# Kernel optimization log

Hardware: AMD Instinct MI355X
Metric: run time of the kernel (lower is better)

## Reference

```python
import jax, jax.numpy as jnp
import numpy as np

N = 100000   # nodes
E = 1600000  # edges
IN_CH = 128
EDGE_DIM = 16
HEADS = 4
OUT_CH = 16
NEG_SLOPE = 0.2


def setup_inputs() -> dict:
    key = jax.random.key(0)
    ks = jax.random.split(key, 12)
    HC = HEADS * OUT_CH
    inp = {
        "x": jax.random.normal(ks[0], (N, IN_CH), dtype=jnp.float32),
        "edge_index": jax.random.randint(ks[1], (2, E), 0, N, dtype=jnp.int32),
        "edge_attr": jax.random.normal(ks[2], (E, EDGE_DIM), dtype=jnp.float32),
        # linear layer params (W stored as [in, out] so y = x @ W + b)
        "W_src": jax.random.normal(ks[3], (IN_CH, HC), dtype=jnp.float32) / np.sqrt(IN_CH),
        "b_src": jnp.zeros((HC,), dtype=jnp.float32),
        "W_dst": jax.random.normal(ks[4], (IN_CH, HC), dtype=jnp.float32) / np.sqrt(IN_CH),
        "b_dst": jnp.zeros((HC,), dtype=jnp.float32),
        "W_edge": jax.random.normal(ks[5], (EDGE_DIM, HC), dtype=jnp.float32) / np.sqrt(EDGE_DIM),
        "b_edge": jnp.zeros((HC,), dtype=jnp.float32),
        # attention vectors [1, heads, out_channels]
        "att_src": jax.random.normal(ks[6], (1, HEADS, OUT_CH), dtype=jnp.float32) * 0.1,
        "att_dst": jax.random.normal(ks[7], (1, HEADS, OUT_CH), dtype=jnp.float32) * 0.1,
        "att_edge": jax.random.normal(ks[8], (1, HEADS, OUT_CH), dtype=jnp.float32) * 0.1,
    }
    return inp


def _segment_softmax(alpha, seg, num_segments):
    # alpha: [E, H]; softmax over edges sharing the same dst node (seg).
    m = jax.ops.segment_max(alpha, seg, num_segments=num_segments)
    m = jnp.where(jnp.isfinite(m), m, 0.0)  # empty segments -> -inf; neutralize
    a = jnp.exp(alpha - m[seg])
    s = jax.ops.segment_sum(a, seg, num_segments=num_segments)
    return a / (s[seg] + 1e-16)


def reference(x, edge_index, edge_attr, W_src, b_src, W_dst, b_dst,
              W_edge, b_edge, att_src, att_dst, att_edge):
    n = x.shape[0]
    src_idx, dst_idx = edge_index[0], edge_index[1]

    src = (x @ W_src + b_src).reshape(n, HEADS, OUT_CH)        # [N,H,C]
    dst = (x @ W_dst + b_dst).reshape(n, HEADS, OUT_CH)        # [N,H,C]
    edge_feat = (edge_attr @ W_edge + b_edge).reshape(-1, HEADS, OUT_CH)  # [E,H,C]

    alpha_src = jnp.sum(src * att_src, axis=-1)[src_idx]       # [E,H]
    alpha_dst = jnp.sum(dst * att_dst, axis=-1)[dst_idx]       # [E,H]
    alpha_edge = jnp.sum(edge_feat * att_edge, axis=-1)        # [E,H]

    alpha = alpha_src + alpha_dst + alpha_edge
    alpha = jnp.where(alpha >= 0, alpha, NEG_SLOPE * alpha)    # leaky_relu(0.2)
    alpha = _segment_softmax(alpha, dst_idx, n)                # [E,H]
    # dropout is identity in eval mode

    msg = src[src_idx] * alpha[..., None]                      # [E,H,C]
    out = jax.ops.segment_sum(msg, dst_idx, num_segments=n)    # [N,H,C]
    return out.reshape(n, HEADS * OUT_CH)
```

## Files before the change

### kernel.cpp

```cpp
#include <hip/hip_runtime.h>


#define N_NODES 100000
#define N_EDGES 1600000
#define SCAN_B 1024
#define SCAN_NBLK ((N_NODES + SCAN_B - 1) / SCAN_B)

typedef float f32x4 __attribute__((ext_vector_type(4)));
typedef int   i32x4 __attribute__((ext_vector_type(4)));

static __device__ __forceinline__ unsigned int f2bf(float f) {
    unsigned int u = __float_as_uint(f);
    return (u + 0x7fffu + ((u >> 16) & 1u)) >> 16;
}
static __device__ __forceinline__ float bf2f(unsigned int bits16) {
    return __uint_as_float(bits16 << 16);
}

__global__ __launch_bounds__(256) void k_node_proj(
    const float* __restrict__ x, const float* __restrict__ Wsrc,
    const float* __restrict__ bsrc, const float* __restrict__ Wdst,
    const float* __restrict__ bdst, const float* __restrict__ att_src,
    const float* __restrict__ att_dst, unsigned short* __restrict__ spbf,
    float* __restrict__ alpha_sn, float* __restrict__ alpha_dn)
{
    __shared__ float wS[128 * 64];
    __shared__ float wD[128 * 64];
    const int tid = threadIdx.x;
    const int nbase = blockIdx.x * 32;

    {
        const f32x4* s4 = (const f32x4*)Wsrc;
        const f32x4* d4 = (const f32x4*)Wdst;
        f32x4* ls = (f32x4*)wS;
        f32x4* ld = (f32x4*)wD;
#pragma unroll
        for (int i = 0; i < 8; ++i) {
            ls[tid + i * 256] = s4[tid + i * 256];
            ld[tid + i * 256] = d4[tid + i * 256];
        }
    }
    __syncthreads();

    const int col = tid & 63;
    const int g = tid >> 6;
    const float* xrow = x + (size_t)(nbase + g * 8) * 128;

    float accS[8], accD[8];
#pragma unroll
    for (int i = 0; i < 8; ++i) { accS[i] = 0.f; accD[i] = 0.f; }

    for (int k4 = 0; k4 < 128; k4 += 4) {
        f32x4 xv[8];
#pragma unroll
        for (int i = 0; i < 8; ++i)
            xv[i] = *(const f32x4*)&xrow[i * 128 + k4];
#pragma unroll
        for (int kk = 0; kk < 4; ++kk) {
            const float wsv = wS[(k4 + kk) * 64 + col];
            const float wdv = wD[(k4 + kk) * 64 + col];
#pragma unroll
            for (int i = 0; i < 8; ++i) {
                accS[i] = fmaf(xv[i][kk], wsv, accS[i]);
                accD[i] = fmaf(xv[i][kk], wdv, accD[i]);
            }
        }
    }

    const float bs = bsrc[col], bd = bdst[col];
    const float as_ = att_src[col], ad_ = att_dst[col];
    const int h = col >> 4;
#pragma unroll
    for (int i = 0; i < 8; ++i) {
        const int n = nbase + g * 8 + i;
        float vS = accS[i] + bs;
        float vD = accD[i] + bd;
        spbf[(size_t)n * 64 + col] = (unsigned short)f2bf(vS);
        float t1 = vS * as_;
        float t2 = vD * ad_;
#pragma unroll
        for (int off = 8; off >= 1; off >>= 1) {
            t1 += __shfl_xor(t1, off, 16);
            t2 += __shfl_xor(t2, off, 16);
        }
        if ((col & 15) == 0) {
            alpha_sn[n * 4 + h] = t1;
            alpha_dn[n * 4 + h] = t2;
        }
    }
}

__global__ void k_prep(const float* __restrict__ We, const float* __restrict__ be,
                       const float* __restrict__ att_e, float* __restrict__ V)
{
    const int t = threadIdx.x;
    const int k = t >> 2, h = t & 3;
    float acc = 0.f;
    for (int c = 0; c < 16; ++c)
        acc += We[k * 64 + h * 16 + c] * att_e[h * 16 + c];
    V[k * 4 + h] = acc;
    if (t < 4) {
        float b = 0.f;
        for (int c = 0; c < 16; ++c)
            b += be[t * 16 + c] * att_e[t * 16 + c];
        V[64 + t] = b;
    }
}

__global__ __launch_bounds__(256) void k_hist(const int* __restrict__ ei,
                                               int* __restrict__ cnt)
{
    const int e = blockIdx.x * 256 + threadIdx.x;
    if (e >= N_EDGES) return;
    atomicAdd(&cnt[ei[N_EDGES + e]], 1);
}

__global__ __launch_bounds__(256) void k_scan_part(const int* __restrict__ cnt,
                                                    int* __restrict__ partial)
{
    __shared__ int red[4];
    const int t = threadIdx.x;
    const int base = blockIdx.x * SCAN_B + t * 4;
    int s = 0;
#pragma unroll
    for (int i = 0; i < 4; ++i) {
        const int idx = base + i;
        if (idx < N_NODES) s += cnt[idx];
    }
#pragma unroll
    for (int off = 32; off >= 1; off >>= 1)
        s += __shfl_xor(s, off, 64);
    if ((t & 63) == 0) red[t >> 6] = s;
    __syncthreads();
    if (t == 0)
        partial[blockIdx.x] = red[0] + red[1] + red[2] + red[3];
}

__global__ __launch_bounds__(128) void k_scan_top(int* __restrict__ partial)
{
    __shared__ int sums[128];
    const int t = threadIdx.x;
    sums[t] = (t < SCAN_NBLK) ? partial[t] : 0;
    __syncthreads();
#pragma unroll
    for (int off = 1; off < 128; off <<= 1) {
        int v = (t >= off) ? sums[t - off] : 0;
        __syncthreads();
        sums[t] += v;
        __syncthreads();
    }
    if (t < SCAN_NBLK) partial[t] = (t == 0) ? 0 : sums[t - 1];
}

__global__ __launch_bounds__(256) void k_scan_down(
    const int* __restrict__ cnt, const int* __restrict__ partial,
    int* __restrict__ row_start, int* __restrict__ cursor)
{
    __shared__ int tsum[256];
    const int t = threadIdx.x;
    const int base = blockIdx.x * SCAN_B + t * 4;
    int c[4];
#pragma unroll
    for (int i = 0; i < 4; ++i) {
        const int idx = base + i;
        c[i] = (idx < N_NODES) ? cnt[idx] : 0;
    }
    const int tot = c[0] + c[1] + c[2] + c[3];
    tsum[t] = tot;
    __syncthreads();
#pragma unroll
    for (int off = 1; off < 256; off <<= 1) {
        int v = (t >= off) ? tsum[t - off] : 0;
        __syncthreads();
        tsum[t] += v;
        __syncthreads();
    }
    int run = partial[blockIdx.x] + ((t == 0) ? 0 : tsum[t - 1]);
#pragma unroll
    for (int i = 0; i < 4; ++i) {
        const int idx = base + i;
        if (idx < N_NODES) {
            row_start[idx] = run;
            cursor[idx] = run;
        }
        run += c[i];
    }
    if (blockIdx.x == 0 && t == 0)
        row_start[N_NODES] = N_EDGES;
}

__global__ __launch_bounds__(256) void k_fill(
    const int* __restrict__ ei, const float* __restrict__ ea,
    const float* __restrict__ V, const float* __restrict__ alpha_sn,
    const float* __restrict__ alpha_dn, int* __restrict__ cursor,
    int4* __restrict__ rec)
{
    __shared__ float Vs[68];
    if (threadIdx.x < 68) Vs[threadIdx.x] = V[threadIdx.x];
    __syncthreads();

    const int e = blockIdx.x * 256 + threadIdx.x;
    if (e >= N_EDGES) return;
    const int src = ei[e];
    const int dst = ei[N_EDGES + e];

    const f32x4* ea4 = (const f32x4*)(ea + (size_t)e * 16);
    float ek[16];
    {
        f32x4 c0 = __builtin_nontemporal_load(ea4 + 0);
        f32x4 c1 = __builtin_nontemporal_load(ea4 + 1);
        f32x4 c2 = __builtin_nontemporal_load(ea4 + 2);
        f32x4 c3 = __builtin_nontemporal_load(ea4 + 3);
        ek[0]=c0.x; ek[1]=c0.y; ek[2]=c0.z; ek[3]=c0.w;
        ek[4]=c1.x; ek[5]=c1.y; ek[6]=c1.z; ek[7]=c1.w;
        ek[8]=c2.x; ek[9]=c2.y; ek[10]=c2.z; ek[11]=c2.w;
        ek[12]=c3.x; ek[13]=c3.y; ek[14]=c3.z; ek[15]=c3.w;
    }
    float a[4] = {Vs[64], Vs[65], Vs[66], Vs[67]};
#pragma unroll
    for (int k = 0; k < 16; ++k) {
#pragma unroll
        for (int h = 0; h < 4; ++h)
            a[h] = fmaf(ek[k], Vs[k * 4 + h], a[h]);
    }

    const float4 asn = *(const float4*)(alpha_sn + (size_t)src * 4);
    const float4 adn = *(const float4*)(alpha_dn + (size_t)dst * 4);
    float a0 = a[0] + asn.x + adn.x;
    float a1 = a[1] + asn.y + adn.y;
    float a2 = a[2] + asn.z + adn.z;
    float a3 = a[3] + asn.w + adn.w;
    a0 = (a0 >= 0.f) ? a0 : 0.2f * a0;
    a1 = (a1 >= 0.f) ? a1 : 0.2f * a1;
    a2 = (a2 >= 0.f) ? a2 : 0.2f * a2;
    a3 = (a3 >= 0.f) ? a3 : 0.2f * a3;

    const unsigned int w01 = f2bf(__expf(a0)) | (f2bf(__expf(a1)) << 16);
    const unsigned int w23 = f2bf(__expf(a2)) | (f2bf(__expf(a3)) << 16);

    const int slot = atomicAdd(&cursor[dst], 1);
    i32x4 r;
    r.x = src; r.y = (int)w01; r.z = (int)w23; r.w = 0;
    __builtin_nontemporal_store(r, (i32x4*)&rec[slot]);
}

__global__ __launch_bounds__(256) void k_gather(
    const int* __restrict__ row_start, const int4* __restrict__ rec,
    const unsigned short* __restrict__ spbf, float* __restrict__ out)
{
    const int lane = threadIdx.x & 63;
    const int node = (blockIdx.x * 256 + threadIdx.x) >> 6;
    const int h = lane >> 4;
    const int base = row_start[node];
    const int end = row_start[node + 1];
    const i32x4* rec4 = (const i32x4*)rec;

    float acc = 0.f, denom = 0.f;
    int j = base;
    for (; j + 4 <= end; j += 4) {
        const i32x4 r0 = __builtin_nontemporal_load(rec4 + j);
        const i32x4 r1 = __builtin_nontemporal_load(rec4 + j + 1);
        const i32x4 r2 = __builtin_nontemporal_load(rec4 + j + 2);
        const i32x4 r3 = __builtin_nontemporal_load(rec4 + j + 3);
        const float v0 = bf2f(spbf[((size_t)r0.x << 6) + lane]);
        const float v1 = bf2f(spbf[((size_t)r1.x << 6) + lane]);
        const float v2 = bf2f(spbf[((size_t)r2.x << 6) + lane]);
        const float v3 = bf2f(spbf[((size_t)r3.x << 6) + lane]);
#define WEXT(r) bf2f(((h & 1) ? ((unsigned int)((h < 2) ? r.y : r.z) >> 16) \
                              : ((unsigned int)((h < 2) ? r.y : r.z) & 0xffffu)))
        const float w0 = WEXT(r0), w1 = WEXT(r1), w2 = WEXT(r2), w3 = WEXT(r3);
        denom += (w0 + w1) + (w2 + w3);
        acc = fmaf(w0, v0, acc);
        acc = fmaf(w1, v1, acc);
        acc = fmaf(w2, v2, acc);
        acc = fmaf(w3, v3, acc);
    }
    for (; j < end; ++j) {
        const i32x4 r0 = __builtin_nontemporal_load(rec4 + j);
        const float v0 = bf2f(spbf[((size_t)r0.x << 6) + lane]);
        const float w0 = WEXT(r0);
        denom += w0;
        acc = fmaf(w0, v0, acc);
    }
#undef WEXT
    __builtin_nontemporal_store(acc / (denom + 1e-16f), &out[(size_t)node * 64 + lane]);
}

extern "C" void kernel_launch(void* const* d_in, const int* in_sizes, int n_in,
                              void* d_out, int out_size, void* d_ws, size_t ws_size,
                              hipStream_t stream) {
    const float* x     = (const float*)d_in[0];
    const int*   ei    = (const int*)d_in[1];
    const float* ea    = (const float*)d_in[2];
    const float* Wsrc  = (const float*)d_in[3];
    const float* bsrc  = (const float*)d_in[4];
    const float* Wdst  = (const float*)d_in[5];
    const float* bdst  = (const float*)d_in[6];
    const float* We    = (const float*)d_in[7];
    const float* be    = (const float*)d_in[8];
    const float* att_s = (const float*)d_in[9];
    const float* att_d = (const float*)d_in[10];
    const float* att_e = (const float*)d_in[11];
    float* out = (float*)d_out;

    int4*  rec       = (int4*)d_ws;
    unsigned short* spbf = (unsigned short*)(rec + N_EDGES);
    float* alpha_sn  = (float*)(spbf + (size_t)N_NODES * 64);
    float* alpha_dn  = alpha_sn + (size_t)N_NODES * 4;
    int*   cnt       = (int*)(alpha_dn + (size_t)N_NODES * 4);
    int*   row_start = cnt + N_NODES;
    int*   cursor    = row_start + N_NODES + 4;
    int*   partial   = cursor + N_NODES;
    float* V         = (float*)(partial + 128);

    hipMemsetAsync(cnt, 0, (size_t)N_NODES * sizeof(int), stream);

    k_node_proj<<<N_NODES / 32, 256, 0, stream>>>(x, Wsrc, bsrc, Wdst, bdst,
                                                  att_s, att_d, spbf,
                                                  alpha_sn, alpha_dn);
    k_prep<<<1, 64, 0, stream>>>(We, be, att_e, V);
    k_hist<<<N_EDGES / 256, 256, 0, stream>>>(ei, cnt);
    k_scan_part<<<SCAN_NBLK, 256, 0, stream>>>(cnt, partial);
    k_scan_top<<<1, 128, 0, stream>>>(partial);
    k_scan_down<<<SCAN_NBLK, 256, 0, stream>>>(cnt, partial, row_start, cursor);
    k_fill<<<N_EDGES / 256, 256, 0, stream>>>(ei, ea, V, alpha_sn, alpha_dn,
                                              cursor, rec);
    k_gather<<<(N_NODES + 3) / 4, 256, 0, stream>>>(row_start, rec, spbf, out);
}
```

Before: 578.7 us.

## Fold dst projection into attention vector and stage x in LDS

The full dst projection (x @ W_dst) is replaced by a precomputed 128x4 vector W_dst·att_dst built in k_prep, so alpha_dst becomes a short dot product per node. The node projection kernel no longer stages both weight matrices in LDS. It stages the 32-row x tile in padded shared memory and reads W_src directly from global/cache. This halves the FMA work and shrinks LDS use, which should raise occupancy, at the cost of uncached-in-LDS weight reads and an extra ordering dependency on k_prep.

```diff
diff --git a/kernel.cpp b/kernel.cpp
--- a/kernel.cpp
+++ b/kernel.cpp
@@ -17,94 +17,121 @@
     return __uint_as_float(bits16 << 16);
 }
 
+__global__ __launch_bounds__(640) void k_prep(
+    const float* __restrict__ We, const float* __restrict__ be,
+    const float* __restrict__ att_e, const float* __restrict__ Wdst,
+    const float* __restrict__ bdst, const float* __restrict__ att_d,
+    float* __restrict__ V)
+{
+    const int t = threadIdx.x;
+    if (t < 64) {
+        const int k = t >> 2, h = t & 3;
+        float acc = 0.f;
+        for (int c = 0; c < 16; ++c)
+            acc += We[k * 64 + h * 16 + c] * att_e[h * 16 + c];
+        V[k * 4 + h] = acc;
+        if (t < 4) {
+            float b = 0.f;
+            for (int c = 0; c < 16; ++c)
+                b += be[t * 16 + c] * att_e[t * 16 + c];
+            V[64 + t] = b;
+        }
+    } else if (t < 576) {
+        const int j = t - 64;
+        const int k = j >> 2, h = j & 3;
+        float acc = 0.f;
+        for (int c = 0; c < 16; ++c)
+            acc += Wdst[k * 64 + h * 16 + c] * att_d[h * 16 + c];
+        V[68 + j] = acc;
+    } else if (t < 580) {
+        const int h = t - 576;
+        float b = 0.f;
+        for (int c = 0; c < 16; ++c)
+            b += bdst[h * 16 + c] * att_d[h * 16 + c];
+        V[580 + h] = b;
+    }
+}
+
 __global__ __launch_bounds__(256) void k_node_proj(
     const float* __restrict__ x, const float* __restrict__ Wsrc,
-    const float* __restrict__ bsrc, const float* __restrict__ Wdst,
-    const float* __restrict__ bdst, const float* __restrict__ att_src,
-    const float* __restrict__ att_dst, unsigned short* __restrict__ spbf,
+    const float* __restrict__ bsrc, const float* __restrict__ att_src,
+    const float* __restrict__ Vbuf, unsigned short* __restrict__ spbf,
     float* __restrict__ alpha_sn, float* __restrict__ alpha_dn)
 {
-    __shared__ float wS[128 * 64];
-    __shared__ float wD[128 * 64];
+    __shared__ float xs[32 * 132];
+    __shared__ float uDs[4 * 132];
+    __shared__ float bDs[4];
     const int tid = threadIdx.x;
     const int nbase = blockIdx.x * 32;
 
     {
-        const f32x4* s4 = (const f32x4*)Wsrc;
-        const f32x4* d4 = (const f32x4*)Wdst;
-        f32x4* ls = (f32x4*)wS;
-        f32x4* ld = (f32x4*)wD;
-#pragma unroll
-        for (int i = 0; i < 8; ++i) {
-            ls[tid + i * 256] = s4[tid + i * 256];
-            ld[tid + i * 256] = d4[tid + i * 256];
-        }
+        const f32x4* xsrc = (const f32x4*)(x + (size_t)nbase * 128);
+#pragma unroll
+        for (int i = 0; i < 4; ++i) {
+            const int idx = tid + i * 256;
+            const int n = idx >> 5, q = idx & 31;
+            *(f32x4*)&xs[n * 132 + q * 4] = xsrc[idx];
+        }
+#pragma unroll
+        for (int i = 0; i < 2; ++i) {
+            const int j = tid + i * 256;
+            const int k = j >> 2, h = j & 3;
+            uDs[h * 132 + k] = Vbuf[68 + j];
+        }
+        if (tid < 4) bDs[tid] = Vbuf[580 + tid];
     }
     __syncthreads();
 
     const int col = tid & 63;
     const int g = tid >> 6;
-    const float* xrow = x + (size_t)(nbase + g * 8) * 128;
-
-    float accS[8], accD[8];
-#pragma unroll
-    for (int i = 0; i < 8; ++i) { accS[i] = 0.f; accD[i] = 0.f; }
+
+    float accS[8];
+#pragma unroll
+    for (int i = 0; i < 8; ++i) accS[i] = 0.f;
 
     for (int k4 = 0; k4 < 128; k4 += 4) {
         f32x4 xv[8];
 #pragma unroll
         for (int i = 0; i < 8; ++i)
-            xv[i] = *(const f32x4*)&xrow[i * 128 + k4];
+            xv[i] = *(const f32x4*)&xs[(g * 8 + i) * 132 + k4];
 #pragma unroll
         for (int kk = 0; kk < 4; ++kk) {
-            const float wsv = wS[(k4 + kk) * 64 + col];
-            const float wdv = wD[(k4 + kk) * 64 + col];
-#pragma unroll
-            for (int i = 0; i < 8; ++i) {
+            const float wsv = Wsrc[(k4 + kk) * 64 + col];
+#pragma unroll
+            for (int i = 0; i < 8; ++i)
                 accS[i] = fmaf(xv[i][kk], wsv, accS[i]);
-                accD[i] = fmaf(xv[i][kk], wdv, accD[i]);
-            }
-        }
-    }
-
-    const float bs = bsrc[col], bd = bdst[col];
-    const float as_ = att_src[col], ad_ = att_dst[col];
+        }
+    }
+
+    const int li = col & 7, lh = (col >> 3) & 3, khalf = (col >> 5) * 64;
+    float ad = 0.f;
+#pragma unroll
+    for (int kq = 0; kq < 16; ++kq) {
+        const f32x4 xq = *(const f32x4*)&xs[(g * 8 + li) * 132 + khalf + kq * 4];
+        const f32x4 uq = *(const f32x4*)&uDs[lh * 132 + khalf + kq * 4];
+#pragma unroll
+        for (int j = 0; j < 4; ++j)
+            ad = fmaf(xq[j], uq[j], ad);
+    }
+    ad += __shfl_xor(ad, 32);
+
+    const float bs = bsrc[col];
+    const float as_ = att_src[col];
     const int h = col >> 4;
 #pragma unroll
     for (int i = 0; i < 8; ++i) {
         const int n = nbase + g * 8 + i;
-        float vS = accS[i] + bs;
-        float vD = accD[i] + bd;
+        const float vS = accS[i] + bs;
         spbf[(size_t)n * 64 + col] = (unsigned short)f2bf(vS);
         float t1 = vS * as_;
-        float t2 = vD * ad_;
-#pragma unroll
-        for (int off = 8; off >= 1; off >>= 1) {
+#pragma unroll
+        for (int off = 8; off >= 1; off >>= 1)
             t1 += __shfl_xor(t1, off, 16);
-            t2 += __shfl_xor(t2, off, 16);
-        }
-        if ((col & 15) == 0) {
+        if ((col & 15) == 0)
             alpha_sn[n * 4 + h] = t1;
-            alpha_dn[n * 4 + h] = t2;
-        }
-    }
-}
-
-__global__ void k_prep(const float* __restrict__ We, const float* __restrict__ be,
-                       const float* __restrict__ att_e, float* __restrict__ V)
-{
-    const int t = threadIdx.x;
-    const int k = t >> 2, h = t & 3;
-    float acc = 0.f;
-    for (int c = 0; c < 16; ++c)
-        acc += We[k * 64 + h * 16 + c] * att_e[h * 16 + c];
-    V[k * 4 + h] = acc;
-    if (t < 4) {
-        float b = 0.f;
-        for (int c = 0; c < 16; ++c)
-            b += be[t * 16 + c] * att_e[t * 16 + c];
-        V[64 + t] = b;
-    }
+    }
+    if (col < 32)
+        alpha_dn[(nbase + g * 8 + li) * 4 + lh] = ad + bDs[lh];
 }
 
 __global__ __launch_bounds__(256) void k_hist(const int* __restrict__ ei,
@@ -315,10 +342,9 @@
 
     hipMemsetAsync(cnt, 0, (size_t)N_NODES * sizeof(int), stream);
 
-    k_node_proj<<<N_NODES / 32, 256, 0, stream>>>(x, Wsrc, bsrc, Wdst, bdst,
-                                                  att_s, att_d, spbf,
-                                                  alpha_sn, alpha_dn);
-    k_prep<<<1, 64, 0, stream>>>(We, be, att_e, V);
+    k_prep<<<1, 640, 0, stream>>>(We, be, att_e, Wdst, bdst, att_d, V);
+    k_node_proj<<<N_NODES / 32, 256, 0, stream>>>(x, Wsrc, bsrc, att_s, V,
+                                                  spbf, alpha_sn, alpha_dn);
     k_hist<<<N_EDGES / 256, 256, 0, stream>>>(ei, cnt);
     k_scan_part<<<SCAN_NBLK, 256, 0, stream>>>(cnt, partial);
     k_scan_top<<<1, 128, 0, stream>>>(partial);
```

After: 496.6 us. 1.17x faster.
